# Kernel tuning notes

Hardware: AMD Instinct MI355X
Metric: run time of the kernel (lower is better)

Reference implementation:

```python
import jax, jax.numpy as jnp
import numpy as np

FMAP = 5
C = 2048
NC = 201  # n_classes + 1


def _conv(x, w, stride, pad):
    return jax.lax.conv_general_dilated(
        x, w, (stride, stride), [(pad, pad), (pad, pad)],
        dimension_numbers=('NCHW', 'OIHW', 'NCHW'))


def _bn(x, g, b, eps=1e-5):
    # training-mode batch norm (batch statistics), as in the torch forward
    m = x.mean((0, 2, 3), keepdims=True)
    v = x.var((0, 2, 3), keepdims=True)
    return (x - m) / jnp.sqrt(v + eps) * g[None, :, None, None] + b[None, :, None, None]


def _grid_sample(img, grid):
    # img [B,C,H,W]; grid [B,K,2] normalized coords (x,y), align_corners=True,
    # bilinear, zero padding -> [B,C,K]
    B, Ch, H, W = img.shape
    gx = (grid[..., 0] + 1.0) * 0.5 * (W - 1)
    gy = (grid[..., 1] + 1.0) * 0.5 * (H - 1)
    x0 = jnp.floor(gx); y0 = jnp.floor(gy)
    x1 = x0 + 1.0; y1 = y0 + 1.0
    wx1 = gx - x0; wx0 = 1.0 - wx1
    wy1 = gy - y0; wy0 = 1.0 - wy1
    imgf = img.reshape(B, Ch, H * W)

    def gather(xi, yi):
        valid = (xi >= 0) & (xi <= W - 1) & (yi >= 0) & (yi <= H - 1)
        xi_ = jnp.clip(xi, 0, W - 1).astype(jnp.int32)
        yi_ = jnp.clip(yi, 0, H - 1).astype(jnp.int32)
        idx = yi_ * W + xi_  # [B,K]
        v = jnp.take_along_axis(imgf, idx[:, None, :], axis=2)  # [B,C,K]
        return v * valid[:, None, :].astype(img.dtype)

    out = (gather(x0, y0) * (wx0 * wy0)[:, None, :]
           + gather(x1, y0) * (wx1 * wy0)[:, None, :]
           + gather(x0, y1) * (wx0 * wy1)[:, None, :]
           + gather(x1, y1) * (wx1 * wy1)[:, None, :])
    return out


def setup_inputs() -> dict:
    key = jax.random.key(0)
    ks = jax.random.split(key, 12)
    B = 8
    return {
        'x': jax.random.normal(ks[0], (B, C, 10, 10), jnp.float32),
        'epoch': 1,
        'flag': 0,
        'conv_last_w': jax.random.normal(ks[1], (C, C, 3, 3), jnp.float32) * 0.02,
        'bn_last_g': jnp.ones((C,), jnp.float32),
        'bn_last_b': jnp.zeros((C,), jnp.float32),
        'loc_w1': jax.random.normal(ks[2], (C, C, 3, 3), jnp.float32) * 0.02,
        'loc_g1': jnp.ones((C,), jnp.float32),
        'loc_b1': jnp.zeros((C,), jnp.float32),
        'loc_w2': jax.random.normal(ks[3], (C, C, 3, 3), jnp.float32) * 0.02,
        'loc_g2': jnp.ones((C,), jnp.float32),
        'loc_b2': jnp.zeros((C,), jnp.float32),
        'fc1_w': jax.random.normal(ks[4], (512, C * 9), jnp.float32) * 0.02,
        'fc2_w': jax.random.normal(ks[5], (4, 512), jnp.float32) * 0.001,
        'conv_stn_w': jax.random.normal(ks[6], (NC, C, 3, 3), jnp.float32) * 0.02,
        'conv_stn_b': jnp.zeros((NC,), jnp.float32),
    }


def reference(x, epoch, flag, conv_last_w, bn_last_g, bn_last_b,
              loc_w1, loc_g1, loc_b1, loc_w2, loc_g2, loc_b2,
              fc1_w, fc2_w, conv_stn_w, conv_stn_b):
    B = x.shape[0]
    # backbone tail: conv_last (s=2, pad=1) + bn_last -> [B,2048,5,5]
    f = _bn(_conv(x, conv_last_w, 2, 1), bn_last_g, bn_last_b)

    # localization network (conv-bn-relu x2, pad=1) -> [B,2048,5,5]
    xs = jax.nn.relu(_bn(_conv(f, loc_w1, 1, 1), loc_g1, loc_b1))
    xs = jax.nn.relu(_bn(_conv(xs, loc_w2, 1, 1), loc_g2, loc_b2))
    xs_p = jnp.pad(xs, ((0, 0), (0, 0), (1, 1), (1, 1)))  # [B,2048,7,7]

    # batched per-cell fc_loc: 25 overlapping 3x3 patches (i outer, j inner)
    patches = jnp.stack([xs_p[:, :, i:i + 3, j:j + 3]
                         for i in range(FMAP) for j in range(FMAP)], axis=1)
    patches = patches.reshape(B, FMAP * FMAP, C * 9)  # (C, kh, kw) flatten order
    h = jax.nn.relu(jnp.einsum('bpf,hf->bph', patches, fc1_w))
    p = jnp.einsum('bph,oh->bpo', h, fc2_w)  # [B,25,4]

    # theta = [[1+p0, 0, p1], [0, 1+p2, p3]]
    zero = jnp.zeros_like(p[..., 0])
    row0 = jnp.stack([1.0 + p[..., 0], zero, p[..., 1]], -1)
    row1 = jnp.stack([zero, 1.0 + p[..., 2], p[..., 3]], -1)
    theta = jnp.stack([row0, row1], -2)  # [B,25,2,3]

    # identity affine grid on padded 7x7 map (align_corners=True), 3x3 windows
    lin = jnp.linspace(-1.0, 1.0, FMAP + 2)
    gxm, gym = jnp.meshgrid(lin, lin, indexing='xy')  # gxm[y,x]=lin[x]
    base = jnp.stack([gxm, gym], -1)  # [7,7,2]
    pos = jnp.stack([base[i:i + 3, j:j + 3]
                     for i in range(FMAP) for j in range(FMAP)], 0)
    pos_h = jnp.concatenate([pos.reshape(25, 9, 2), jnp.ones((25, 9, 1))], -1)

    # transformed sampling grids: pos_hom @ theta^T -> [B,25,9,2]
    grids = jnp.einsum('pkc,bpdc->bpkd', pos_h, theta).reshape(B, 25 * 9, 2)

    # batched grid_sample of padded features, then stitch 25 3x3 tiles -> 15x15
    f_p = jnp.pad(f, ((0, 0), (0, 0), (1, 1), (1, 1)))  # [B,2048,7,7]
    samp = _grid_sample(f_p, grids)  # [B,C,225]
    temp = samp.reshape(B, C, FMAP, FMAP, 3, 3).transpose(0, 1, 2, 4, 3, 5)
    temp = temp.reshape(B, C, 3 * FMAP, 3 * FMAP)  # [B,2048,15,15]

    # conv_stn (k=3, s=3) -> [B,201,5,5]; joint softmax over class x position
    out = _conv(temp, conv_stn_w, 3, 0) + conv_stn_b[None, :, None, None]
    s = jax.nn.softmax(out.reshape(B, -1), axis=1).reshape(B, NC, FMAP, FMAP)
    classif_scores = s.sum((2, 3))  # [B,201]
    return classif_scores, s, theta.reshape(B * 25, 2, 3)
```

## Files before the change

kernel.cpp:

```cpp
#include <hip/hip_runtime.h>
#include <hip/hip_bf16.h>


#define GK 18432
#define GN 200
#define NPAD 256

typedef __attribute__((ext_vector_type(8))) short bf16x8;
typedef __attribute__((ext_vector_type(4))) float f32x4;
typedef unsigned int u32;

__global__ __launch_bounds__(256) void im2col_bf16(
    const float* __restrict__ in, __hip_bfloat16* __restrict__ Bt,
    int H, int stride, int pad)
{
    int tid = blockIdx.x * 256 + threadIdx.x;
    int n = tid / GK;
    int k = tid - n * GK;
    float v = 0.f;
    if (n < GN) {
        int c = k / 9; int r9 = k - c * 9;
        int kh = r9 / 3, kw = r9 - kh * 3;
        int b = n / 25; int pp = n - b * 25;
        int oh = pp / 5, ow = pp - oh * 5;
        int r = oh * stride + kh - pad;
        int s = ow * stride + kw - pad;
        if (r >= 0 && r < H && s >= 0 && s < H)
            v = in[(((b * 2048 + c) * H) + r) * H + s];
    }
    Bt[tid] = __float2bfloat16(v);
}

__global__ __launch_bounds__(256) void gridsample_bf16(
    const float* __restrict__ f, const float* __restrict__ gridb,
    __hip_bfloat16* __restrict__ Bt)
{
    int tid = blockIdx.x * 256 + threadIdx.x;
    int n = tid / GK;
    int cq = tid - n * GK;
    float v = 0.f;
    if (n < GN) {
        int c = cq / 9, q = cq - c * 9;
        int b = n / 25, p = n - b * 25;
        int g = (b * 225 + p * 9 + q) * 2;
        float px = gridb[g], py = gridb[g + 1];
        float x0f = floorf(px), y0f = floorf(py);
        int x0 = (int)x0f, y0 = (int)y0f;
        float wx1 = px - x0f, wx0 = 1.f - wx1;
        float wy1 = py - y0f, wy0 = 1.f - wy1;
        const float* fb = f + ((size_t)b * 2048 + c) * 25;
        auto fetch = [&](int xi, int yi) -> float {
            if (xi < 1 || xi > 5 || yi < 1 || yi > 5) return 0.f;
            return fb[(yi - 1) * 5 + (xi - 1)];
        };
        v = fetch(x0, y0) * wx0 * wy0
          + fetch(x0 + 1, y0) * wx1 * wy0
          + fetch(x0, y0 + 1) * wx0 * wy1
          + fetch(x0 + 1, y0 + 1) * wx1 * wy1;
    }
    Bt[tid] = __float2bfloat16(v);
}

__global__ __launch_bounds__(256) void gemm_mfma(
    const float* __restrict__ A, const __hip_bfloat16* __restrict__ Bt,
    float* __restrict__ C, int M, int kchunk)
{
    __shared__ unsigned short As[128 * 40];
    __shared__ unsigned short Bs[128 * 32];

    const int tid = threadIdx.x;
    const int bn = blockIdx.x * 128;
    const int bm = blockIdx.y * 128;
    const int kbase = blockIdx.z * kchunk;

    const int wave = tid >> 6, lane = tid & 63;
    const int wm = (wave & 1) * 64, wn = (wave >> 1) * 64;
    const int lm = lane & 15, lq = lane >> 4;

    const int arow = tid >> 1;
    const int akh = (tid & 1) * 16;
    const bool aok = (bm + arow) < M;
    const float* aptr = A + (size_t)(bm + arow) * GK + kbase + akh;
    uint4* awr = (uint4*)&As[arow * 40 + akh];

    const int brow = wave * 32 + (lane >> 2);
    const int bkoff = (lane & 3) * 8;
    const __hip_bfloat16* bptr0 = Bt + (size_t)(bn + brow) * GK + kbase + bkoff;
    const __hip_bfloat16* bptr1 = bptr0 + (size_t)16 * GK;
    unsigned short* bwr0 = &Bs[wave * 1024];
    unsigned short* bwr1 = &Bs[wave * 1024 + 512];

    f32x4 acc[4][4] = {};

    for (int k0 = 0; k0 < kchunk; k0 += 32) {
        __builtin_amdgcn_global_load_lds((const u32*)(bptr0 + k0), (u32*)bwr0, 16, 0, 0);
        __builtin_amdgcn_global_load_lds((const u32*)(bptr1 + k0), (u32*)bwr1, 16, 0, 0);

        u32 pk[8];
        if (aok) {
            const float4* ap = (const float4*)(aptr + k0);
            float4 a0 = ap[0], a1 = ap[1], a2 = ap[2], a3 = ap[3];
            pk[0] = __builtin_amdgcn_perm(__float_as_uint(a0.y), __float_as_uint(a0.x), 0x07060302u);
            pk[1] = __builtin_amdgcn_perm(__float_as_uint(a0.w), __float_as_uint(a0.z), 0x07060302u);
            pk[2] = __builtin_amdgcn_perm(__float_as_uint(a1.y), __float_as_uint(a1.x), 0x07060302u);
            pk[3] = __builtin_amdgcn_perm(__float_as_uint(a1.w), __float_as_uint(a1.z), 0x07060302u);
            pk[4] = __builtin_amdgcn_perm(__float_as_uint(a2.y), __float_as_uint(a2.x), 0x07060302u);
            pk[5] = __builtin_amdgcn_perm(__float_as_uint(a2.w), __float_as_uint(a2.z), 0x07060302u);
            pk[6] = __builtin_amdgcn_perm(__float_as_uint(a3.y), __float_as_uint(a3.x), 0x07060302u);
            pk[7] = __builtin_amdgcn_perm(__float_as_uint(a3.w), __float_as_uint(a3.z), 0x07060302u);
        } else {
#pragma unroll
            for (int i = 0; i < 8; ++i) pk[i] = 0;
        }
        awr[0] = make_uint4(pk[0], pk[1], pk[2], pk[3]);
        awr[1] = make_uint4(pk[4], pk[5], pk[6], pk[7]);

        __syncthreads();

        bf16x8 af[4], bfr[4];
#pragma unroll
        for (int i = 0; i < 4; ++i) {
            af[i]  = *(const bf16x8*)&As[(wm + i * 16 + lm) * 40 + lq * 8];
            bfr[i] = *(const bf16x8*)&Bs[(wn + i * 16 + lm) * 32 + lq * 8];
        }
#pragma unroll
        for (int i = 0; i < 4; ++i)
#pragma unroll
            for (int j = 0; j < 4; ++j)
                acc[i][j] = __builtin_amdgcn_mfma_f32_16x16x32_bf16(
                    af[i], bfr[j], acc[i][j], 0, 0, 0);

        __syncthreads();
    }

#pragma unroll
    for (int i = 0; i < 4; ++i) {
        int row0 = bm + wm + i * 16 + lq * 4;
#pragma unroll
        for (int j = 0; j < 4; ++j) {
            int col = bn + wn + j * 16 + lm;
            if (col < GN) {
#pragma unroll
                for (int r = 0; r < 4; ++r)
                    if (row0 + r < M)
                        atomicAdd(&C[(size_t)(row0 + r) * GN + col], acc[i][j][r]);
            }
        }
    }
}

__global__ void bnstats_kernel(const float* __restrict__ y,
                               float* __restrict__ meanb,
                               float* __restrict__ rstdb)
{
    int ch = blockIdx.x;
    int lane = threadIdx.x;
    const float* p = y + (size_t)ch * GN;
    float s = 0.f, sq = 0.f;
    for (int idx = lane; idx < GN; idx += 64) {
        float v = p[idx];
        s += v; sq += v * v;
    }
    for (int off = 32; off; off >>= 1) {
        s += __shfl_down(s, off);
        sq += __shfl_down(sq, off);
    }
    if (lane == 0) {
        float m = s * (1.f / 200.f);
        float var = sq * (1.f / 200.f) - m * m;
        meanb[ch] = m;
        rstdb[ch] = rsqrtf(var + 1e-5f);
    }
}

__global__ __launch_bounds__(256) void bn_apply_kernel(
    const float* __restrict__ y, const float* __restrict__ meanb,
    const float* __restrict__ rstdb, const float* __restrict__ g,
    const float* __restrict__ bb, float* __restrict__ out, int relu)
{
    int tid = blockIdx.x * 256 + threadIdx.x;
    if (tid >= 409600) return;
    int b = tid / (2048 * 25);
    int rem = tid % (2048 * 25);
    int c = rem / 25;
    int pp = rem % 25;
    float v = y[(size_t)c * GN + b * 25 + pp];
    v = (v - meanb[c]) * rstdb[c] * g[c] + bb[c];
    if (relu) v = fmaxf(v, 0.f);
    out[tid] = v;
}

__global__ void fc2_kernel(const float* __restrict__ hmat,
                           const float* __restrict__ fc2w,
                           float* __restrict__ pbuf)
{
    int n = blockIdx.x;
    int oo = threadIdx.x >> 6;
    int lane = threadIdx.x & 63;
    float s = 0.f;
#pragma unroll
    for (int j = 0; j < 8; ++j) {
        int hh = lane + 64 * j;
        s += fmaxf(hmat[(size_t)hh * GN + n], 0.f) * fc2w[oo * 512 + hh];
    }
    for (int off = 32; off; off >>= 1) s += __shfl_down(s, off);
    if (lane == 0) pbuf[n * 4 + oo] = s;
}

__global__ void theta_grids_kernel(const float* __restrict__ pbuf,
                                   float* __restrict__ gridb,
                                   float* __restrict__ outT)
{
    int tid = blockIdx.x * 256 + threadIdx.x;
    if (tid >= 1800) return;
    int b = tid / 225;
    int rem = tid % 225;
    int p = rem / 9;
    int k = rem % 9;
    int i = p / 5, j = p % 5;
    int dy = k / 3, dx = k % 3;
    int n = b * 25 + p;
    float p0 = pbuf[n * 4 + 0];
    float p1 = pbuf[n * 4 + 1];
    float p2 = pbuf[n * 4 + 2];
    float p3 = pbuf[n * 4 + 3];
    float x = (float)(j + dx) * (1.f / 3.f) - 1.f;
    float y = (float)(i + dy) * (1.f / 3.f) - 1.f;
    float gx = (1.f + p0) * x + p1;
    float gy = (1.f + p2) * y + p3;
    gridb[tid * 2 + 0] = (gx + 1.f) * 3.f;
    gridb[tid * 2 + 1] = (gy + 1.f) * 3.f;
    if (k == 0) {
        outT[n * 6 + 0] = 1.f + p0;
        outT[n * 6 + 1] = 0.f;
        outT[n * 6 + 2] = p1;
        outT[n * 6 + 3] = 0.f;
        outT[n * 6 + 4] = 1.f + p2;
        outT[n * 6 + 5] = p3;
    }
}

__global__ void softmax_kernel(const float* __restrict__ stn,
                               const float* __restrict__ bias,
                               float* __restrict__ outC,
                               float* __restrict__ outS)
{
    int b = blockIdx.x;
    __shared__ float red[256];
    int t = threadIdx.x;

    float mx = -1e30f;
    for (int idx = t; idx < 5025; idx += 256) {
        int o = idx / 25, pp = idx % 25;
        mx = fmaxf(mx, stn[(size_t)o * GN + b * 25 + pp] + bias[o]);
    }
    red[t] = mx; __syncthreads();
    for (int s = 128; s; s >>= 1) {
        if (t < s) red[t] = fmaxf(red[t], red[t + s]);
        __syncthreads();
    }
    mx = red[0]; __syncthreads();

    float sm = 0.f;
    for (int idx = t; idx < 5025; idx += 256) {
        int o = idx / 25, pp = idx % 25;
        sm += expf(stn[(size_t)o * GN + b * 25 + pp] + bias[o] - mx);
    }
    red[t] = sm; __syncthreads();
    for (int s = 128; s; s >>= 1) {
        if (t < s) red[t] += red[t + s];
        __syncthreads();
    }
    float inv = 1.f / red[0];

    for (int idx = t; idx < 5025; idx += 256) {
        int o = idx / 25, pp = idx % 25;
        outS[b * 5025 + idx] =
            expf(stn[(size_t)o * GN + b * 25 + pp] + bias[o] - mx) * inv;
    }
    for (int o = t; o < 201; o += 256) {
        float cs = 0.f;
        for (int pp = 0; pp < 25; ++pp)
            cs += expf(stn[(size_t)o * GN + b * 25 + pp] + bias[o] - mx);
        outC[b * 201 + o] = cs * inv;
    }
}

extern "C" void kernel_launch(void* const* d_in, const int* in_sizes, int n_in,
                              void* d_out, int out_size, void* d_ws, size_t ws_size,
                              hipStream_t stream)
{
    const float* x           = (const float*)d_in[0];
    const float* conv_last_w = (const float*)d_in[3];
    const float* bn_last_g   = (const float*)d_in[4];
    const float* bn_last_b   = (const float*)d_in[5];
    const float* loc_w1      = (const float*)d_in[6];
    const float* loc_g1      = (const float*)d_in[7];
    const float* loc_b1      = (const float*)d_in[8];
    const float* loc_w2      = (const float*)d_in[9];
    const float* loc_g2      = (const float*)d_in[10];
    const float* loc_b2      = (const float*)d_in[11];
    const float* fc1_w       = (const float*)d_in[12];
    const float* fc2_w       = (const float*)d_in[13];
    const float* conv_stn_w  = (const float*)d_in[14];
    const float* conv_stn_b  = (const float*)d_in[15];

    __hip_bfloat16* Bt = (__hip_bfloat16*)d_ws;
    float* fp    = (float*)((char*)d_ws + (size_t)NPAD * GK * 2);
    float* t1    = fp;
    float* fbuf  = t1 + 409600;
    float* xs1   = fbuf + 409600;
    float* xs    = xs1 + 409600;
    float* hmat  = xs + 409600;
    float* stn   = hmat + 102400;
    float* pbuf  = stn + 40200;
    float* gridb = pbuf + 800;
    float* meanb = gridb + 3600;
    float* rstdb = meanb + 2048;

    float* outC = (float*)d_out;
    float* outS = outC + 8 * 201;
    float* outT = outS + 8 * 201 * 25;

    dim3 b256(256);
    const int nB = (NPAD * GK) / 256;

    im2col_bf16<<<nB, b256, 0, stream>>>(x, Bt, 10, 2, 1);
    hipMemsetAsync(t1, 0, 409600 * sizeof(float), stream);
    gemm_mfma<<<dim3(2, 16, 16), b256, 0, stream>>>(conv_last_w, Bt, t1, 2048, GK / 16);
    bnstats_kernel<<<2048, 64, 0, stream>>>(t1, meanb, rstdb);
    bn_apply_kernel<<<1600, b256, 0, stream>>>(t1, meanb, rstdb, bn_last_g, bn_last_b, fbuf, 0);

    im2col_bf16<<<nB, b256, 0, stream>>>(fbuf, Bt, 5, 1, 1);
    hipMemsetAsync(t1, 0, 409600 * sizeof(float), stream);
    gemm_mfma<<<dim3(2, 16, 16), b256, 0, stream>>>(loc_w1, Bt, t1, 2048, GK / 16);
    bnstats_kernel<<<2048, 64, 0, stream>>>(t1, meanb, rstdb);
    bn_apply_kernel<<<1600, b256, 0, stream>>>(t1, meanb, rstdb, loc_g1, loc_b1, xs1, 1);

    im2col_bf16<<<nB, b256, 0, stream>>>(xs1, Bt, 5, 1, 1);
    hipMemsetAsync(t1, 0, 409600 * sizeof(float), stream);
    gemm_mfma<<<dim3(2, 16, 16), b256, 0, stream>>>(loc_w2, Bt, t1, 2048, GK / 16);
    bnstats_kernel<<<2048, 64, 0, stream>>>(t1, meanb, rstdb);
    bn_apply_kernel<<<1600, b256, 0, stream>>>(t1, meanb, rstdb, loc_g2, loc_b2, xs, 1);

    im2col_bf16<<<nB, b256, 0, stream>>>(xs, Bt, 5, 1, 1);
    hipMemsetAsync(hmat, 0, 102400 * sizeof(float), stream);
    gemm_mfma<<<dim3(2, 4, 32), b256, 0, stream>>>(fc1_w, Bt, hmat, 512, GK / 32);

    fc2_kernel<<<200, 256, 0, stream>>>(hmat, fc2_w, pbuf);
    theta_grids_kernel<<<8, 256, 0, stream>>>(pbuf, gridb, outT);

    gridsample_bf16<<<nB, b256, 0, stream>>>(fbuf, gridb, Bt);

    hipMemsetAsync(stn, 0, 40200 * sizeof(float), stream);
    gemm_mfma<<<dim3(2, 2, 32), b256, 0, stream>>>(conv_stn_w, Bt, stn, 201, GK / 32);

    softmax_kernel<<<8, 256, 0, stream>>>(stn, conv_stn_b, outC, outS);
}
```

Measured before the change: 779.3 us.

## Double-buffer GEMM LDS, fuse BN kernels, vectorize im2col, batch memsets, widen split-K

The GEMM now double-buffers its A and B shared-memory tiles, prefetching the next K slice while the current one feeds MFMA, and sets launch bounds for three blocks per CU. The BN stats and apply kernels are merged into one per-channel kernel, removing a launch and the extra pass over memory. im2col and gridsample now write eight bf16 values per thread with a single 16-byte store. The four separate memsets become one up front, using separate output buffers. Split-K factors are raised to 24, 48 and 96 to launch more blocks, at the cost of more atomic traffic.

```diff
diff --git a/kernel.cpp b/kernel.cpp
--- a/kernel.cpp
+++ b/kernel.cpp
@@ -5,73 +5,93 @@
 #define GK 18432
 #define GN 200
 #define NPAD 256
+#define GK8 (GK / 8)
 
 typedef __attribute__((ext_vector_type(8))) short bf16x8;
 typedef __attribute__((ext_vector_type(4))) float f32x4;
 typedef unsigned int u32;
+typedef unsigned short u16;
+
+static __device__ __forceinline__ u16 f2bf(float v) {
+    __hip_bfloat16 h = __float2bfloat16(v);
+    return *(u16*)&h;
+}
 
 __global__ __launch_bounds__(256) void im2col_bf16(
-    const float* __restrict__ in, __hip_bfloat16* __restrict__ Bt,
+    const float* __restrict__ in, u16* __restrict__ Bt,
     int H, int stride, int pad)
 {
     int tid = blockIdx.x * 256 + threadIdx.x;
-    int n = tid / GK;
-    int k = tid - n * GK;
-    float v = 0.f;
+    int n = tid / GK8;
+    int k0 = (tid - n * GK8) * 8;
+    u16 o[8] = {0, 0, 0, 0, 0, 0, 0, 0};
     if (n < GN) {
-        int c = k / 9; int r9 = k - c * 9;
-        int kh = r9 / 3, kw = r9 - kh * 3;
-        int b = n / 25; int pp = n - b * 25;
+        int b = n / 25, pp = n - b * 25;
         int oh = pp / 5, ow = pp - oh * 5;
-        int r = oh * stride + kh - pad;
-        int s = ow * stride + kw - pad;
-        if (r >= 0 && r < H && s >= 0 && s < H)
-            v = in[(((b * 2048 + c) * H) + r) * H + s];
-    }
-    Bt[tid] = __float2bfloat16(v);
+        int rb = oh * stride - pad, sb = ow * stride - pad;
+        const float* inb = in + (size_t)b * 2048 * H * H;
+#pragma unroll
+        for (int j = 0; j < 8; ++j) {
+            int k = k0 + j;
+            int c = k / 9; int r9 = k - c * 9;
+            int kh = r9 / 3, kw = r9 - kh * 3;
+            int r = rb + kh, s = sb + kw;
+            float v = 0.f;
+            if ((unsigned)r < (unsigned)H && (unsigned)s < (unsigned)H)
+                v = inb[(c * H + r) * H + s];
+            o[j] = f2bf(v);
+        }
+    }
+    *(uint4*)&Bt[(size_t)tid * 8] = *(const uint4*)o;
 }
 
 __global__ __launch_bounds__(256) void gridsample_bf16(
     const float* __restrict__ f, const float* __restrict__ gridb,
-    __hip_bfloat16* __restrict__ Bt)
+    u16* __restrict__ Bt)
 {
     int tid = blockIdx.x * 256 + threadIdx.x;
-    int n = tid / GK;
-    int cq = tid - n * GK;
-    float v = 0.f;
+    int n = tid / GK8;
+    int k0 = (tid - n * GK8) * 8;
+    u16 o[8] = {0, 0, 0, 0, 0, 0, 0, 0};
     if (n < GN) {
-        int c = cq / 9, q = cq - c * 9;
         int b = n / 25, p = n - b * 25;
-        int g = (b * 225 + p * 9 + q) * 2;
-        float px = gridb[g], py = gridb[g + 1];
-        float x0f = floorf(px), y0f = floorf(py);
-        int x0 = (int)x0f, y0 = (int)y0f;
-        float wx1 = px - x0f, wx0 = 1.f - wx1;
-        float wy1 = py - y0f, wy0 = 1.f - wy1;
-        const float* fb = f + ((size_t)b * 2048 + c) * 25;
-        auto fetch = [&](int xi, int yi) -> float {
-            if (xi < 1 || xi > 5 || yi < 1 || yi > 5) return 0.f;
-            return fb[(yi - 1) * 5 + (xi - 1)];
-        };
-        v = fetch(x0, y0) * wx0 * wy0
-          + fetch(x0 + 1, y0) * wx1 * wy0
-          + fetch(x0, y0 + 1) * wx0 * wy1
-          + fetch(x0 + 1, y0 + 1) * wx1 * wy1;
-    }
-    Bt[tid] = __float2bfloat16(v);
-}
-
-__global__ __launch_bounds__(256) void gemm_mfma(
+        const float* gb = gridb + (b * 225 + p * 9) * 2;
+#pragma unroll
+        for (int j = 0; j < 8; ++j) {
+            int k = k0 + j;
+            int c = k / 9, q = k - c * 9;
+            float px = gb[q * 2], py = gb[q * 2 + 1];
+            float x0f = floorf(px), y0f = floorf(py);
+            int x0 = (int)x0f, y0 = (int)y0f;
+            float wx1 = px - x0f, wx0 = 1.f - wx1;
+            float wy1 = py - y0f, wy0 = 1.f - wy1;
+            const float* fb = f + ((size_t)b * 2048 + c) * 25;
+            auto fetch = [&](int xi, int yi) -> float {
+                if (xi < 1 || xi > 5 || yi < 1 || yi > 5) return 0.f;
+                return fb[(yi - 1) * 5 + (xi - 1)];
+            };
+            float v = fetch(x0, y0) * wx0 * wy0
+                    + fetch(x0 + 1, y0) * wx1 * wy0
+                    + fetch(x0, y0 + 1) * wx0 * wy1
+                    + fetch(x0 + 1, y0 + 1) * wx1 * wy1;
+            o[j] = f2bf(v);
+        }
+    }
+    *(uint4*)&Bt[(size_t)tid * 8] = *(const uint4*)o;
+}
+
+__global__ __launch_bounds__(256, 3) void gemm_mfma(
     const float* __restrict__ A, const __hip_bfloat16* __restrict__ Bt,
     float* __restrict__ C, int M, int kchunk)
 {
-    __shared__ unsigned short As[128 * 40];
-    __shared__ unsigned short Bs[128 * 32];
+    __shared__ u16 As[2][128 * 40];
+    __shared__ u16 Bs[2][128 * 32];
 
     const int tid = threadIdx.x;
     const int bn = blockIdx.x * 128;
     const int bm = blockIdx.y * 128;
     const int kbase = blockIdx.z * kchunk;
+    const int iters = kchunk >> 5;
 
     const int wave = tid >> 6, lane = tid & 63;
     const int wm = (wave & 1) * 64, wn = (wave >> 1) * 64;
@@ -81,47 +101,66 @@
     const int akh = (tid & 1) * 16;
     const bool aok = (bm + arow) < M;
     const float* aptr = A + (size_t)(bm + arow) * GK + kbase + akh;
-    uint4* awr = (uint4*)&As[arow * 40 + akh];
 
     const int brow = wave * 32 + (lane >> 2);
     const int bkoff = (lane & 3) * 8;
     const __hip_bfloat16* bptr0 = Bt + (size_t)(bn + brow) * GK + kbase + bkoff;
     const __hip_bfloat16* bptr1 = bptr0 + (size_t)16 * GK;
-    unsigned short* bwr0 = &Bs[wave * 1024];
-    unsigned short* bwr1 = &Bs[wave * 1024 + 512];
 
     f32x4 acc[4][4] = {};
 
-    for (int k0 = 0; k0 < kchunk; k0 += 32) {
-        __builtin_amdgcn_global_load_lds((const u32*)(bptr0 + k0), (u32*)bwr0, 16, 0, 0);
-        __builtin_amdgcn_global_load_lds((const u32*)(bptr1 + k0), (u32*)bwr1, 16, 0, 0);
-
-        u32 pk[8];
+#define PACK_WRITE(buf, r0, r1, r2, r3)                                        \
+    {                                                                          \
+        uint4* awr = (uint4*)&As[buf][arow * 40 + akh];                        \
+        awr[0] = make_uint4(                                                   \
+            __builtin_amdgcn_perm(__float_as_uint(r0.y), __float_as_uint(r0.x), 0x07060302u), \
+            __builtin_amdgcn_perm(__float_as_uint(r0.w), __float_as_uint(r0.z), 0x07060302u), \
+            __builtin_amdgcn_perm(__float_as_uint(r1.y), __float_as_uint(r1.x), 0x07060302u), \
+            __builtin_amdgcn_perm(__float_as_uint(r1.w), __float_as_uint(r1.z), 0x07060302u));\
+        awr[1] = make_uint4(                                                   \
+            __builtin_amdgcn_perm(__float_as_uint(r2.y), __float_as_uint(r2.x), 0x07060302u), \
+            __builtin_amdgcn_perm(__float_as_uint(r2.w), __float_as_uint(r2.z), 0x07060302u), \
+            __builtin_amdgcn_perm(__float_as_uint(r3.y), __float_as_uint(r3.x), 0x07060302u), \
+            __builtin_amdgcn_perm(__float_as_uint(r3.w), __float_as_uint(r3.z), 0x07060302u));\
+    }
+
+    __builtin_amdgcn_global_load_lds((const u32*)bptr0, (u32*)&Bs[0][wave * 1024], 16, 0, 0);
+    __builtin_amdgcn_global_load_lds((const u32*)bptr1, (u32*)&Bs[0][wave * 1024 + 512], 16, 0, 0);
+    {
+        float4 a0, a1, a2, a3;
         if (aok) {
-            const float4* ap = (const float4*)(aptr + k0);
-            float4 a0 = ap[0], a1 = ap[1], a2 = ap[2], a3 = ap[3];
-            pk[0] = __builtin_amdgcn_perm(__float_as_uint(a0.y), __float_as_uint(a0.x), 0x07060302u);
-            pk[1] = __builtin_amdgcn_perm(__float_as_uint(a0.w), __float_as_uint(a0.z), 0x07060302u);
-            pk[2] = __builtin_amdgcn_perm(__float_as_uint(a1.y), __float_as_uint(a1.x), 0x07060302u);
-            pk[3] = __builtin_amdgcn_perm(__float_as_uint(a1.w), __float_as_uint(a1.z), 0x07060302u);
-            pk[4] = __builtin_amdgcn_perm(__float_as_uint(a2.y), __float_as_uint(a2.x), 0x07060302u);
-            pk[5] = __builtin_amdgcn_perm(__float_as_uint(a2.w), __float_as_uint(a2.z), 0x07060302u);
-            pk[6] = __builtin_amdgcn_perm(__float_as_uint(a3.y), __float_as_uint(a3.x), 0x07060302u);
-            pk[7] = __builtin_amdgcn_perm(__float_as_uint(a3.w), __float_as_uint(a3.z), 0x07060302u);
+            const float4* ap = (const float4*)aptr;
+            a0 = ap[0]; a1 = ap[1]; a2 = ap[2]; a3 = ap[3];
         } else {
-#pragma unroll
-            for (int i = 0; i < 8; ++i) pk[i] = 0;
-        }
-        awr[0] = make_uint4(pk[0], pk[1], pk[2], pk[3]);
-        awr[1] = make_uint4(pk[4], pk[5], pk[6], pk[7]);
-
-        __syncthreads();
+            a0 = a1 = a2 = a3 = make_float4(0.f, 0.f, 0.f, 0.f);
+        }
+        PACK_WRITE(0, a0, a1, a2, a3);
+    }
+    __syncthreads();
+
+    for (int k = 0; k < iters; ++k) {
+        const int cur = k & 1, nxt = cur ^ 1;
+        const bool more = (k + 1) < iters;
+        float4 a0, a1, a2, a3;
+        if (more) {
+            const int koff = (k + 1) << 5;
+            __builtin_amdgcn_global_load_lds((const u32*)(bptr0 + koff),
+                                             (u32*)&Bs[nxt][wave * 1024], 16, 0, 0);
+            __builtin_amdgcn_global_load_lds((const u32*)(bptr1 + koff),
+                                             (u32*)&Bs[nxt][wave * 1024 + 512], 16, 0, 0);
+            if (aok) {
+                const float4* ap = (const float4*)(aptr + koff);
+                a0 = ap[0]; a1 = ap[1]; a2 = ap[2]; a3 = ap[3];
+            } else {
+                a0 = a1 = a2 = a3 = make_float4(0.f, 0.f, 0.f, 0.f);
+            }
+        }
 
         bf16x8 af[4], bfr[4];
 #pragma unroll
         for (int i = 0; i < 4; ++i) {
-            af[i]  = *(const bf16x8*)&As[(wm + i * 16 + lm) * 40 + lq * 8];
-            bfr[i] = *(const bf16x8*)&Bs[(wn + i * 16 + lm) * 32 + lq * 8];
+            af[i]  = *(const bf16x8*)&As[cur][(wm + i * 16 + lm) * 40 + lq * 8];
+            bfr[i] = *(const bf16x8*)&Bs[cur][(wn + i * 16 + lm) * 32 + lq * 8];
         }
 #pragma unroll
         for (int i = 0; i < 4; ++i)
@@ -130,6 +169,7 @@
                 acc[i][j] = __builtin_amdgcn_mfma_f32_16x16x32_bf16(
                     af[i], bfr[j], acc[i][j], 0, 0, 0);
 
+        if (more) PACK_WRITE(nxt, a0, a1, a2, a3);
         __syncthreads();
     }
 
@@ -147,11 +187,13 @@
             }
         }
     }
-}
-
-__global__ void bnstats_kernel(const float* __restrict__ y,
-                               float* __restrict__ meanb,
-                               float* __restrict__ rstdb)
+#undef PACK_WRITE
+}
+
+__global__ void bn_fused(const float* __restrict__ y,
+                         const float* __restrict__ g,
+                         const float* __restrict__ bb,
+                         float* __restrict__ out, int relu)
 {
     int ch = blockIdx.x;
     int lane = threadIdx.x;
@@ -165,29 +207,19 @@
         s += __shfl_down(s, off);
         sq += __shfl_down(sq, off);
     }
-    if (lane == 0) {
-        float m = s * (1.f / 200.f);
-        float var = sq * (1.f / 200.f) - m * m;
-        meanb[ch] = m;
-        rstdb[ch] = rsqrtf(var + 1e-5f);
-    }
-}
-
-__global__ __launch_bounds__(256) void bn_apply_kernel(
-    const float* __restrict__ y, const float* __restrict__ meanb,
-    const float* __restrict__ rstdb, const float* __restrict__ g,
-    const float* __restrict__ bb, float* __restrict__ out, int relu)
-{
-    int tid = blockIdx.x * 256 + threadIdx.x;
-    if (tid >= 409600) return;
-    int b = tid / (2048 * 25);
-    int rem = tid % (2048 * 25);
-    int c = rem / 25;
-    int pp = rem % 25;
-    float v = y[(size_t)c * GN + b * 25 + pp];
-    v = (v - meanb[c]) * rstdb[c] * g[c] + bb[c];
-    if (relu) v = fmaxf(v, 0.f);
-    out[tid] = v;
+    s = __shfl(s, 0);
+    sq = __shfl(sq, 0);
+    float m = s * (1.f / 200.f);
+    float var = sq * (1.f / 200.f) - m * m;
+    float rstd = rsqrtf(var + 1e-5f);
+    float sc = rstd * g[ch];
+    float sh = bb[ch] - m * sc;
+    for (int idx = lane; idx < GN; idx += 64) {
+        float v = p[idx] * sc + sh;
+        if (relu) v = fmaxf(v, 0.f);
+        int b = idx / 25, pp = idx - b * 25;
+        out[(size_t)b * 51200 + ch * 25 + pp] = v;
+    }
 }
 
 __global__ void fc2_kernel(const float* __restrict__ hmat,
@@ -305,55 +337,49 @@
     const float* conv_stn_w  = (const float*)d_in[14];
     const float* conv_stn_b  = (const float*)d_in[15];
 
-    __hip_bfloat16* Bt = (__hip_bfloat16*)d_ws;
-    float* fp    = (float*)((char*)d_ws + (size_t)NPAD * GK * 2);
-    float* t1    = fp;
-    float* fbuf  = t1 + 409600;
+    u16* Bt = (u16*)d_ws;
+    float* fp = (float*)((char*)d_ws + (size_t)NPAD * GK * 2);
+    float* t1a  = fp;
+    float* t1b  = t1a + 409600;
+    float* t1c  = t1b + 409600;
+    float* hmat = t1c + 409600;
+    float* stn  = hmat + 102400;
+    float* fbuf  = stn + 40200;
     float* xs1   = fbuf + 409600;
     float* xs    = xs1 + 409600;
-    float* hmat  = xs + 409600;
-    float* stn   = hmat + 102400;
-    float* pbuf  = stn + 40200;
+    float* pbuf  = xs + 409600;
     float* gridb = pbuf + 800;
-    float* meanb = gridb + 3600;
-    float* rstdb = meanb + 2048;
 
     float* outC = (float*)d_out;
     float* outS = outC + 8 * 201;
     float* outT = outS + 8 * 201 * 25;
 
     dim3 b256(256);
-    const int nB = (NPAD * GK) / 256;
+    const int nB = (NPAD * GK / 8) / 256;
+
+    hipMemsetAsync(t1a, 0, (size_t)(409600 * 3 + 102400 + 40200) * sizeof(float), stream);
 
     im2col_bf16<<<nB, b256, 0, stream>>>(x, Bt, 10, 2, 1);
-    hipMemsetAsync(t1, 0, 409600 * sizeof(float), stream);
-    gemm_mfma<<<dim3(2, 16, 16), b256, 0, stream>>>(conv_last_w, Bt, t1, 2048, GK / 16);
-    bnstats_kernel<<<2048, 64, 0, stream>>>(t1, meanb, rstdb);
-    bn_apply_kernel<<<1600, b256, 0, stream>>>(t1, meanb, rstdb, bn_last_g, bn_last_b, fbuf, 0);
+    gemm_mfma<<<dim3(2, 16, 24), b256, 0, stream>>>(conv_last_w, (__hip_bfloat16*)Bt, t1a, 2048, GK / 24);
+    bn_fused<<<2048, 64, 0, stream>>>(t1a, bn_last_g, bn_last_b, fbuf, 0);
 
     im2col_bf16<<<nB, b256, 0, stream>>>(fbuf, Bt, 5, 1, 1);
-    hipMemsetAsync(t1, 0, 409600 * sizeof(float), stream);
-    gemm_mfma<<<dim3(2, 16, 16), b256, 0, stream>>>(loc_w1, Bt, t1, 2048, GK / 16);
-    bnstats_kernel<<<2048, 64, 0, stream>>>(t1, meanb, rstdb);
-    bn_apply_kernel<<<1600, b256, 0, stream>>>(t1, meanb, rstdb, loc_g1, loc_b1, xs1, 1);
+    gemm_mfma<<<dim3(2, 16, 24), b256, 0, stream>>>(loc_w1, (__hip_bfloat16*)Bt, t1b, 2048, GK / 24);
+    bn_fused<<<2048, 64, 0, stream>>>(t1b, loc_g1, loc_b1, xs1, 1);
 
     im2col_bf16<<<nB, b256, 0, stream>>>(xs1, Bt, 5, 1, 1);
-    hipMemsetAsync(t1, 0, 409600 * sizeof(float), stream);
-    gemm_mfma<<<dim3(2, 16, 16), b256, 0, stream>>>(loc_w2, Bt, t1, 2048, GK / 16);
-    bnstats_kernel<<<2048, 64, 0, stream>>>(t1, meanb, rstdb);
-    bn_apply_kernel<<<1600, b256, 0, stream>>>(t1, meanb, rstdb, loc_g2, loc_b2, xs, 1);
+    gemm_mfma<<<dim3(2, 16, 24), b256, 0, stream>>>(loc_w2, (__hip_bfloat16*)Bt, t1c, 2048, GK / 24);
+    bn_fused<<<2048, 64, 0, stream>>>(t1c, loc_g2, loc_b2, xs, 1);
 
     im2col_bf16<<<nB, b256, 0, stream>>>(xs, Bt, 5, 1, 1);
-    hipMemsetAsync(hmat, 0, 102400 * sizeof(float), stream);
-    gemm_mfma<<<dim3(2, 4, 32), b256, 0, stream>>>(fc1_w, Bt, hmat, 512, GK / 32);
+    gemm_mfma<<<dim3(2, 4, 48), b256, 0, stream>>>(fc1_w, (__hip_bfloat16*)Bt, hmat, 512, GK / 48);
 
     fc2_kernel<<<200, 256, 0, stream>>>(hmat, fc2_w, pbuf);
     theta_grids_kernel<<<8, 256, 0, stream>>>(pbuf, gridb, outT);
 
     gridsample_bf16<<<nB, b256, 0, stream>>>(fbuf, gridb, Bt);
 
-    hipMemsetAsync(stn, 0, 40200 * sizeof(float), stream);
-    gemm_mfma<<<dim3(2, 2, 32), b256, 0, stream>>>(conv_stn_w, Bt, stn, 201, GK / 32);
+    gemm_mfma<<<dim3(2, 2, 96), b256, 0, stream>>>(conv_stn_w, (__hip_bfloat16*)Bt, stn, 201, GK / 96);
 
     softmax_kernel<<<8, 256, 0, stream>>>(stn, conv_stn_b, outC, outS);
 }
```

Result: slower. 832.0 us (+6.8%).
